# Kernel optimization log

Measured on AMD Instinct MI355X. Metric: run time of the kernel, lower is better.

The kernel has to match this reference:

```python
import jax, jax.numpy as jnp
import numpy as np

N_NODES = 50000
N_EDGES = 800000
IN_DIM = 256
HID_DIM = 128  # hidden_dim == output_dim (fc2 is applied twice in the original)


def setup_inputs() -> dict:
    key = jax.random.key(0)
    ks = jax.random.split(key, 8)
    x = jax.random.normal(ks[0], (N_NODES, IN_DIM), dtype=jnp.float32)
    W1 = jax.random.normal(ks[1], (IN_DIM, HID_DIM), dtype=jnp.float32) * (1.0 / np.sqrt(IN_DIM))
    b1 = jax.random.normal(ks[2], (HID_DIM,), dtype=jnp.float32) * 0.01
    W2 = jax.random.normal(ks[3], (HID_DIM, HID_DIM), dtype=jnp.float32) * (1.0 / np.sqrt(HID_DIM))
    b2 = jax.random.normal(ks[4], (HID_DIM,), dtype=jnp.float32) * 0.01
    adj_vals = jax.random.uniform(ks[5], (N_EDGES,), dtype=jnp.float32)
    adj_rows = jax.random.randint(ks[6], (N_EDGES,), 0, N_NODES, dtype=jnp.int32)
    adj_cols = jax.random.randint(ks[7], (N_EDGES,), 0, N_NODES, dtype=jnp.int32)
    return {"x": x, "W1": W1, "b1": b1, "W2": W2, "b2": b2,
            "adj_vals": adj_vals, "adj_rows": adj_rows, "adj_cols": adj_cols}


def reference(x, W1, b1, W2, b2, adj_vals, adj_rows, adj_cols):
    # fc1 + ReLU: [N, in] -> [N, hid]
    h = jax.nn.relu(x @ W1 + b1)
    # spmm(adj, h): out[i] = sum over edges (i<-j) vals * h[j]
    msgs = adj_vals[:, None] * h[adj_cols]            # [E, hid] gather
    agg = jax.ops.segment_sum(msgs, adj_rows, num_segments=N_NODES)  # [N, hid]
    # gcn_forward applies fc2, then forward applies fc2 AGAIN (faithful to source)
    h2 = agg @ W2 + b2
    logits = h2 @ W2 + b2
    return jax.nn.softmax(logits, axis=1)
```

## Files before the change

### kernel.cpp

```cpp
#include <hip/hip_runtime.h>
#include <hip/hip_fp16.h>

#define NN 50000
#define EE 800000
#define IND 256
#define HD 128
#define EPB 4096
#define GBLK 196
#define NBIN 196

typedef _Float16 half2v __attribute__((ext_vector_type(2)));
typedef _Float16 half4v __attribute__((ext_vector_type(4)));
typedef _Float16 half8v __attribute__((ext_vector_type(8)));
typedef float f32x4 __attribute__((ext_vector_type(4)));

__global__ __launch_bounds__(128) void w1t_kernel(const float* __restrict__ W1,
                                                  _Float16* __restrict__ W1T) {
  const int k = blockIdx.x;
  const int c = threadIdx.x;
  W1T[c * IND + k] = (_Float16)W1[k * HD + c];
}

__global__ __launch_bounds__(128) void w2sq_kernel(const float* __restrict__ W2,
                                                   const float* __restrict__ b2,
                                                   _Float16* __restrict__ W2sqT,
                                                   float* __restrict__ b2eff) {
  const int r = blockIdx.x;
  const int c = threadIdx.x;
  float acc = 0.f;
#pragma unroll 8
  for (int k = 0; k < HD; ++k)
    acc = fmaf(W2[r * HD + k], W2[k * HD + c], acc);
  W2sqT[c * HD + r] = (_Float16)acc;
  if (r == 0) {
    float be = b2[c];
#pragma unroll 8
    for (int k = 0; k < HD; ++k)
      be = fmaf(b2[k], W2[k * HD + c], be);
    b2eff[c] = be;
  }
}

__global__ __launch_bounds__(256) void fc1_kernel(const float* __restrict__ x,
                                                  const _Float16* __restrict__ W1T,
                                                  const float* __restrict__ b1,
                                                  _Float16* __restrict__ h) {
  __shared__ _Float16 As[64 * 40];
  const int tid = threadIdx.x;
  const int l = tid & 63;
  const int w = tid >> 6;
  const int row0 = blockIdx.x * 64;
  const int lr = l & 15;
  const int lk = l >> 4;

  f32x4 acc[4][2];
#pragma unroll
  for (int mi = 0; mi < 4; ++mi)
#pragma unroll
    for (int ni = 0; ni < 2; ++ni) acc[mi][ni] = (f32x4){0.f, 0.f, 0.f, 0.f};

#pragma unroll 1
  for (int kt = 0; kt < 8; ++kt) {
    const int k0 = kt * 32;
    __syncthreads();
#pragma unroll
    for (int i = 0; i < 2; ++i) {
      const int f = tid + i * 256;
      const int row = f >> 3, kq = f & 7;
      const int rg = min(row0 + row, NN - 1);
      const float4 xv = *(const float4*)&x[(size_t)rg * IND + k0 + kq * 4];
      half4v hv = {(_Float16)xv.x, (_Float16)xv.y, (_Float16)xv.z, (_Float16)xv.w};
      *(half4v*)&As[row * 40 + kq * 4] = hv;
    }
    __syncthreads();
    const half8v b0 = *(const half8v*)&W1T[(size_t)(w * 32 + lr) * IND + k0 + lk * 8];
    const half8v b1f = *(const half8v*)&W1T[(size_t)(w * 32 + 16 + lr) * IND + k0 + lk * 8];
#pragma unroll
    for (int mi = 0; mi < 4; ++mi) {
      const half8v a = *(const half8v*)&As[(mi * 16 + lr) * 40 + lk * 8];
      acc[mi][0] = __builtin_amdgcn_mfma_f32_16x16x32_f16(a, b0, acc[mi][0], 0, 0, 0);
      acc[mi][1] = __builtin_amdgcn_mfma_f32_16x16x32_f16(a, b1f, acc[mi][1], 0, 0, 0);
    }
  }
  const float bias0 = b1[w * 32 + lr];
  const float bias1 = b1[w * 32 + 16 + lr];
#pragma unroll
  for (int mi = 0; mi < 4; ++mi) {
#pragma unroll
    for (int j = 0; j < 4; ++j) {
      const int rg = row0 + mi * 16 + lk * 4 + j;
      if (rg < NN) {
        h[(size_t)rg * HD + w * 32 + lr] = (_Float16)fmaxf(acc[mi][0][j] + bias0, 0.f);
        h[(size_t)rg * HD + w * 32 + 16 + lr] = (_Float16)fmaxf(acc[mi][1][j] + bias1, 0.f);
      }
    }
  }
}

__global__ void hist_kernel(const int* __restrict__ rows, int* __restrict__ counts) {
  int e = blockIdx.x * 256 + threadIdx.x;
  if (e < EE) atomicAdd(&counts[rows[e]], 1);
}

__device__ inline int wave_incl_scan(int v, int lane) {
#pragma unroll
  for (int off = 1; off < 64; off <<= 1) {
    int n = __shfl_up(v, off);
    if (lane >= off) v += n;
  }
  return v;
}

__global__ __launch_bounds__(256) void scan_a_kernel(const int* __restrict__ counts,
                                                     int* __restrict__ incl,
                                                     int* __restrict__ bsum) {
  __shared__ int wtot[4];
  const int t = threadIdx.x;
  const int i = blockIdx.x * 256 + t;
  const int lane = t & 63, wid = t >> 6;
  const int v = (i < NN) ? counts[i] : 0;
  int sc = wave_incl_scan(v, lane);
  if (lane == 63) wtot[wid] = sc;
  __syncthreads();
  int pre = 0;
#pragma unroll
  for (int w = 0; w < 3; ++w) pre += (wid > w) ? wtot[w] : 0;
  if (i < NN) incl[i] = sc + pre;
  if (t == 255) bsum[blockIdx.x] = pre + sc;
}

__global__ __launch_bounds__(256) void scan_b_kernel(int* __restrict__ bsum,
                                                     int* __restrict__ boffs,
                                                     int nblk) {
  __shared__ int wtot[4];
  const int t = threadIdx.x;
  const int lane = t & 63, wid = t >> 6;
  const int v = (t < nblk) ? bsum[t] : 0;
  int sc = wave_incl_scan(v, lane);
  if (lane == 63) wtot[wid] = sc;
  __syncthreads();
  int pre = 0;
#pragma unroll
  for (int w = 0; w < 3; ++w) pre += (wid > w) ? wtot[w] : 0;
  if (t < nblk) boffs[t] = sc + pre - v;
}

__global__ __launch_bounds__(256) void scan_c_kernel(const int* __restrict__ incl,
                                                     const int* __restrict__ boffs,
                                                     int* __restrict__ row_ptr) {
  const int i = blockIdx.x * 256 + threadIdx.x;
  if (i == 0) row_ptr[0] = 0;
  if (i < NN) row_ptr[i + 1] = boffs[blockIdx.x] + incl[i];
}

__global__ __launch_bounds__(256) void count_kernel(const int* __restrict__ rows,
                                                    int* __restrict__ countmat) {
  __shared__ int cnt[NBIN];
  const int t = threadIdx.x, blk = blockIdx.x;
  for (int i = t; i < NBIN; i += 256) cnt[i] = 0;
  __syncthreads();
  const int e0 = blk * EPB;
  const int eN = min(e0 + EPB, EE);
  for (int e = e0 + t; e < eN; e += 256) atomicAdd(&cnt[rows[e] >> 8], 1);
  __syncthreads();
  for (int i = t; i < NBIN; i += 256) countmat[i * GBLK + blk] = cnt[i];
}

__global__ __launch_bounds__(256) void scanmat_kernel(const int* __restrict__ countmat,
                                                      const int* __restrict__ row_ptr,
                                                      int* __restrict__ offmat) {
  __shared__ int wtot[4];
  const int bin = blockIdx.x;
  const int t = threadIdx.x, lane = t & 63, wid = t >> 6;
  const int v = (t < GBLK) ? countmat[bin * GBLK + t] : 0;
  int sc = wave_incl_scan(v, lane);
  if (lane == 63) wtot[wid] = sc;
  __syncthreads();
  int pre = 0;
#pragma unroll
  for (int w = 0; w < 3; ++w) pre += (wid > w) ? wtot[w] : 0;
  const int binbase = row_ptr[bin << 8];
  if (t < GBLK) offmat[bin * GBLK + t] = binbase + pre + sc - v;
}

__global__ __launch_bounds__(256) void scatter_kernel(const int* __restrict__ rows,
                                                      const int* __restrict__ cols,
                                                      const float* __restrict__ vals,
                                                      const int* __restrict__ offmat,
                                                      uint2* __restrict__ edges_b) {
  __shared__ uint2 st[EPB];
  __shared__ unsigned char binof[EPB];
  __shared__ int cnt[NBIN], lofs[NBIN], gbase[NBIN];
  __shared__ int wtot[4];
  const int t = threadIdx.x, blk = blockIdx.x;
  const int lane = t & 63, wid = t >> 6;
  for (int i = t; i < NBIN; i += 256) cnt[i] = 0;
  __syncthreads();
  const int e0 = blk * EPB;
  const int n = min(EPB, EE - e0);
  for (int i = t; i < n; i += 256) atomicAdd(&cnt[rows[e0 + i] >> 8], 1);
  __syncthreads();
  {
    const int v = (t < NBIN) ? cnt[t] : 0;
    int sc = wave_incl_scan(v, lane);
    if (lane == 63) wtot[wid] = sc;
    __syncthreads();
    int pre = 0;
#pragma unroll
    for (int w = 0; w < 3; ++w) pre += (wid > w) ? wtot[w] : 0;
    if (t < NBIN) {
      lofs[t] = pre + sc - v;
      gbase[t] = offmat[t * GBLK + blk];
    }
  }
  __syncthreads();
  for (int i = t; i < NBIN; i += 256) cnt[i] = 0;
  __syncthreads();
  for (int i = t; i < n; i += 256) {
    const int r = rows[e0 + i];
    const int b = r >> 8;
    const int p = atomicAdd(&cnt[b], 1);
    const int j = lofs[b] + p;
    st[j] = make_uint2(__float_as_uint(vals[e0 + i]),
                       ((unsigned)r << 16) | (unsigned)cols[e0 + i]);
    binof[j] = (unsigned char)b;
  }
  __syncthreads();
  for (int j = t; j < n; j += 256) {
    const int b = binof[j];
    edges_b[gbase[b] + (j - lofs[b])] = st[j];
  }
}

__global__ __launch_bounds__(256) void binsort_kernel(const uint2* __restrict__ edges_b,
                                                      const int* __restrict__ row_ptr,
                                                      uint2* __restrict__ edges_s) {
  __shared__ int cur[256];
  const int bin = blockIdx.x;
  const int n0 = bin << 8;
  const int nEnd = min(n0 + 256, NN);
  const int t = threadIdx.x;
  if (n0 + t < nEnd) cur[t] = row_ptr[n0 + t];
  __syncthreads();
  const int s = row_ptr[n0];
  const int eEnd = row_ptr[nEnd];
  for (int i = s + t; i < eEnd; i += 256) {
    const uint2 ed = edges_b[i];
    const int r = (int)(ed.y >> 16);
    const int pos = atomicAdd(&cur[r & 255], 1);
    edges_s[pos] = make_uint2(ed.x, ed.y & 0xFFFFu);
  }
}

__global__ __launch_bounds__(256) void spmm_kernel(const _Float16* __restrict__ h,
                                                   const uint2* __restrict__ edges,
                                                   const int* __restrict__ row_ptr,
                                                   _Float16* __restrict__ agg16) {
  const int wid = threadIdx.x >> 6;
  const int lane = threadIdx.x & 63;
  const int node = blockIdx.x * 4 + wid;
  if (node >= NN) return;
  const int s = row_ptr[node];
  const int e = row_ptr[node + 1];
  const unsigned* __restrict__ hu = (const unsigned*)h;
  float ax = 0.f, ay = 0.f;
  int t = s;
  for (; t + 3 < e; t += 4) {
    const uint2 e0 = edges[t + 0], e1 = edges[t + 1];
    const uint2 e2 = edges[t + 2], e3 = edges[t + 3];
    const unsigned g0 = hu[(size_t)e0.y * 64 + lane];
    const unsigned g1 = hu[(size_t)e1.y * 64 + lane];
    const unsigned g2 = hu[(size_t)e2.y * 64 + lane];
    const unsigned g3 = hu[(size_t)e3.y * 64 + lane];
    const __half2 h0 = *(const __half2*)&g0;
    const __half2 h1 = *(const __half2*)&g1;
    const __half2 h2 = *(const __half2*)&g2;
    const __half2 h3 = *(const __half2*)&g3;
    const float v0 = __uint_as_float(e0.x), v1 = __uint_as_float(e1.x);
    const float v2 = __uint_as_float(e2.x), v3 = __uint_as_float(e3.x);
    ax = fmaf(v0, __low2float(h0), ax); ay = fmaf(v0, __high2float(h0), ay);
    ax = fmaf(v1, __low2float(h1), ax); ay = fmaf(v1, __high2float(h1), ay);
    ax = fmaf(v2, __low2float(h2), ax); ay = fmaf(v2, __high2float(h2), ay);
    ax = fmaf(v3, __low2float(h3), ax); ay = fmaf(v3, __high2float(h3), ay);
  }
  for (; t < e; ++t) {
    const uint2 ee = edges[t];
    const unsigned g = hu[(size_t)ee.y * 64 + lane];
    const __half2 hh = *(const __half2*)&g;
    const float v = __uint_as_float(ee.x);
    ax = fmaf(v, __low2float(hh), ax); ay = fmaf(v, __high2float(hh), ay);
  }
  half2v o = {(_Float16)ax, (_Float16)ay};
  *(half2v*)&agg16[(size_t)node * HD + lane * 2] = o;
}

__global__ __launch_bounds__(256) void fc2sm_kernel(const _Float16* __restrict__ agg16,
                                                    const _Float16* __restrict__ W2sqT,
                                                    const float* __restrict__ b2eff,
                                                    float* __restrict__ out) {
  __shared__ _Float16 As[64 * 136];
  __shared__ float redm[64][4];
  __shared__ float reds[64][4];
  const int tid = threadIdx.x;
  const int l = tid & 63;
  const int w = tid >> 6;
  const int row0 = blockIdx.x * 64;
  const int lr = l & 15;
  const int lk = l >> 4;

#pragma unroll
  for (int i = 0; i < 4; ++i) {
    const int f = tid + i * 256;
    const int row = f >> 4, q = f & 15;
    const int rg = min(row0 + row, NN - 1);
    *(uint4*)&As[row * 136 + q * 8] = *(const uint4*)&agg16[(size_t)rg * HD + q * 8];
  }
  __syncthreads();

  f32x4 acc[4][2];
#pragma unroll
  for (int mi = 0; mi < 4; ++mi)
#pragma unroll
    for (int ni = 0; ni < 2; ++ni) acc[mi][ni] = (f32x4){0.f, 0.f, 0.f, 0.f};

#pragma unroll 2
  for (int kt = 0; kt < 4; ++kt) {
    const int k0 = kt * 32;
    const half8v b0 = *(const half8v*)&W2sqT[(size_t)(w * 32 + lr) * HD + k0 + lk * 8];
    const half8v b1f = *(const half8v*)&W2sqT[(size_t)(w * 32 + 16 + lr) * HD + k0 + lk * 8];
#pragma unroll
    for (int mi = 0; mi < 4; ++mi) {
      const half8v a = *(const half8v*)&As[(mi * 16 + lr) * 136 + k0 + lk * 8];
      acc[mi][0] = __builtin_amdgcn_mfma_f32_16x16x32_f16(a, b0, acc[mi][0], 0, 0, 0);
      acc[mi][1] = __builtin_amdgcn_mfma_f32_16x16x32_f16(a, b1f, acc[mi][1], 0, 0, 0);
    }
  }

  const float be0 = b2eff[w * 32 + lr];
  const float be1 = b2eff[w * 32 + 16 + lr];
#pragma unroll
  for (int mi = 0; mi < 4; ++mi)
#pragma unroll
    for (int j = 0; j < 4; ++j) {
      acc[mi][0][j] += be0;
      acc[mi][1][j] += be1;
    }
#pragma unroll
  for (int mi = 0; mi < 4; ++mi)
#pragma unroll
    for (int j = 0; j < 4; ++j) {
      float v = fmaxf(acc[mi][0][j], acc[mi][1][j]);
      v = fmaxf(v, __shfl_xor(v, 1));
      v = fmaxf(v, __shfl_xor(v, 2));
      v = fmaxf(v, __shfl_xor(v, 4));
      v = fmaxf(v, __shfl_xor(v, 8));
      if (lr == 0) redm[mi * 16 + lk * 4 + j][w] = v;
    }
  __syncthreads();
#pragma unroll
  for (int mi = 0; mi < 4; ++mi)
#pragma unroll
    for (int j = 0; j < 4; ++j) {
      const int row = mi * 16 + lk * 4 + j;
      const float m = fmaxf(fmaxf(redm[row][0], redm[row][1]),
                            fmaxf(redm[row][2], redm[row][3]));
      const float e0 = __expf(acc[mi][0][j] - m);
      const float e1 = __expf(acc[mi][1][j] - m);
      acc[mi][0][j] = e0;
      acc[mi][1][j] = e1;
      float s = e0 + e1;
      s += __shfl_xor(s, 1);
      s += __shfl_xor(s, 2);
      s += __shfl_xor(s, 4);
      s += __shfl_xor(s, 8);
      if (lr == 0) reds[row][w] = s;
    }
  __syncthreads();
#pragma unroll
  for (int mi = 0; mi < 4; ++mi)
#pragma unroll
    for (int j = 0; j < 4; ++j) {
      const int row = mi * 16 + lk * 4 + j;
      const int rg = row0 + row;
      if (rg < NN) {
        const float inv = 1.f / (((reds[row][0] + reds[row][1]) +
                                  (reds[row][2] + reds[row][3])));
        out[(size_t)rg * HD + w * 32 + lr] = acc[mi][0][j] * inv;
        out[(size_t)rg * HD + w * 32 + 16 + lr] = acc[mi][1][j] * inv;
      }
    }
}

extern "C" void kernel_launch(void* const* d_in, const int* in_sizes, int n_in,
                              void* d_out, int out_size, void* d_ws, size_t ws_size,
                              hipStream_t stream) {
  (void)in_sizes; (void)n_in; (void)out_size; (void)ws_size;
  const float* x   = (const float*)d_in[0];
  const float* W1  = (const float*)d_in[1];
  const float* b1  = (const float*)d_in[2];
  const float* W2  = (const float*)d_in[3];
  const float* b2  = (const float*)d_in[4];
  const float* adj_vals = (const float*)d_in[5];
  const int* adj_rows   = (const int*)d_in[6];
  const int* adj_cols   = (const int*)d_in[7];
  float* out = (float*)d_out;

  char* ws = (char*)d_ws;
  _Float16* h      = (_Float16*)ws;
  _Float16* agg16  = (_Float16*)(ws + 12800000);
  _Float16* W1T    = (_Float16*)(ws + 25600000);
  _Float16* W2sqT  = (_Float16*)(ws + 25665536);
  float* b2eff     = (float*)(ws + 25698304);
  int* row_ptr     = (int*)(ws + 25698816);
  int* counts      = (int*)(ws + 25898880);
  int* incl        = (int*)(ws + 26098944);
  int* bsum        = (int*)(ws + 26299008);
  int* boffs       = (int*)(ws + 26300032);
  int* countmat    = (int*)(ws + 26301056);
  int* offmat      = (int*)(ws + 26454720);
  uint2* edges_b   = (uint2*)(ws + 26608384);
  uint2* edges_s   = (uint2*)(ws + 33008384);

  const int nblk = (NN + 255) / 256;

  hipMemsetAsync(counts, 0, NN * sizeof(int), stream);

  w1t_kernel<<<IND, HD, 0, stream>>>(W1, W1T);
  w2sq_kernel<<<HD, HD, 0, stream>>>(W2, b2, W2sqT, b2eff);
  fc1_kernel<<<(NN + 63) / 64, 256, 0, stream>>>(x, W1T, b1, h);
  hist_kernel<<<(EE + 255) / 256, 256, 0, stream>>>(adj_rows, counts);
  scan_a_kernel<<<nblk, 256, 0, stream>>>(counts, incl, bsum);
  scan_b_kernel<<<1, 256, 0, stream>>>(bsum, boffs, nblk);
  scan_c_kernel<<<nblk, 256, 0, stream>>>(incl, boffs, row_ptr);
  count_kernel<<<GBLK, 256, 0, stream>>>(adj_rows, countmat);
  scanmat_kernel<<<NBIN, 256, 0, stream>>>(countmat, row_ptr, offmat);
  scatter_kernel<<<GBLK, 256, 0, stream>>>(adj_rows, adj_cols, adj_vals, offmat, edges_b);
  binsort_kernel<<<NBIN, 256, 0, stream>>>(edges_b, row_ptr, edges_s);
  spmm_kernel<<<(NN + 3) / 4, 256, 0, stream>>>(h, edges_s, row_ptr, agg16);
  fc2sm_kernel<<<(NN + 63) / 64, 256, 0, stream>>>(agg16, W2sqT, b2eff, out);
}
```

Measured before the change: 254.5 us.

## Replace full CSR build with 64-row bins and LDS-atomic binned SpMM

Drops the per-node histogram, three-stage scan and the second bin-sort pass. Edges are now bucketed only into 64-row bins (782 bins), using a two-level scan of per-block counts. A new SpMM kernel processes one bin per block and accumulates into a 64x128 fp32 shared-memory tile with LDS atomics, keyed by the local row stored in the packed edge word. This removes several kernel launches and a full edge-array read/write pass, at the cost of shared-memory float atomics in the aggregation, which may contend and add float-ordering nondeterminism.

New measurement: 850.1 us. 234% more time.

```diff
diff --git a/kernel.cpp b/kernel.cpp
--- a/kernel.cpp
+++ b/kernel.cpp
@@ -7,7 +7,7 @@
 #define HD 128
 #define EPB 4096
 #define GBLK 196
-#define NBIN 196
+#define NB 782
 
 typedef _Float16 half2v __attribute__((ext_vector_type(2)));
 typedef _Float16 half4v __attribute__((ext_vector_type(4)));
@@ -97,11 +97,6 @@
   }
 }
 
-__global__ void hist_kernel(const int* __restrict__ rows, int* __restrict__ counts) {
-  int e = blockIdx.x * 256 + threadIdx.x;
-  if (e < EE) atomicAdd(&counts[rows[e]], 1);
-}
-
 __device__ inline int wave_incl_scan(int v, int lane) {
 #pragma unroll
   for (int off = 1; off < 64; off <<= 1) {
@@ -111,64 +106,22 @@
   return v;
 }
 
-__global__ __launch_bounds__(256) void scan_a_kernel(const int* __restrict__ counts,
-                                                     int* __restrict__ incl,
-                                                     int* __restrict__ bsum) {
-  __shared__ int wtot[4];
-  const int t = threadIdx.x;
-  const int i = blockIdx.x * 256 + t;
-  const int lane = t & 63, wid = t >> 6;
-  const int v = (i < NN) ? counts[i] : 0;
-  int sc = wave_incl_scan(v, lane);
-  if (lane == 63) wtot[wid] = sc;
-  __syncthreads();
-  int pre = 0;
-#pragma unroll
-  for (int w = 0; w < 3; ++w) pre += (wid > w) ? wtot[w] : 0;
-  if (i < NN) incl[i] = sc + pre;
-  if (t == 255) bsum[blockIdx.x] = pre + sc;
-}
-
-__global__ __launch_bounds__(256) void scan_b_kernel(int* __restrict__ bsum,
-                                                     int* __restrict__ boffs,
-                                                     int nblk) {
-  __shared__ int wtot[4];
-  const int t = threadIdx.x;
-  const int lane = t & 63, wid = t >> 6;
-  const int v = (t < nblk) ? bsum[t] : 0;
-  int sc = wave_incl_scan(v, lane);
-  if (lane == 63) wtot[wid] = sc;
-  __syncthreads();
-  int pre = 0;
-#pragma unroll
-  for (int w = 0; w < 3; ++w) pre += (wid > w) ? wtot[w] : 0;
-  if (t < nblk) boffs[t] = sc + pre - v;
-}
-
-__global__ __launch_bounds__(256) void scan_c_kernel(const int* __restrict__ incl,
-                                                     const int* __restrict__ boffs,
-                                                     int* __restrict__ row_ptr) {
-  const int i = blockIdx.x * 256 + threadIdx.x;
-  if (i == 0) row_ptr[0] = 0;
-  if (i < NN) row_ptr[i + 1] = boffs[blockIdx.x] + incl[i];
-}
-
 __global__ __launch_bounds__(256) void count_kernel(const int* __restrict__ rows,
                                                     int* __restrict__ countmat) {
-  __shared__ int cnt[NBIN];
+  __shared__ int cnt[NB];
   const int t = threadIdx.x, blk = blockIdx.x;
-  for (int i = t; i < NBIN; i += 256) cnt[i] = 0;
+  for (int i = t; i < NB; i += 256) cnt[i] = 0;
   __syncthreads();
   const int e0 = blk * EPB;
   const int eN = min(e0 + EPB, EE);
-  for (int e = e0 + t; e < eN; e += 256) atomicAdd(&cnt[rows[e] >> 8], 1);
-  __syncthreads();
-  for (int i = t; i < NBIN; i += 256) countmat[i * GBLK + blk] = cnt[i];
-}
-
-__global__ __launch_bounds__(256) void scanmat_kernel(const int* __restrict__ countmat,
-                                                      const int* __restrict__ row_ptr,
-                                                      int* __restrict__ offmat) {
+  for (int e = e0 + t; e < eN; e += 256) atomicAdd(&cnt[rows[e] >> 6], 1);
+  __syncthreads();
+  for (int i = t; i < NB; i += 256) countmat[i * GBLK + blk] = cnt[i];
+}
+
+__global__ __launch_bounds__(256) void scanwithin_kernel(const int* __restrict__ countmat,
+                                                         int* __restrict__ within,
+                                                         int* __restrict__ bintot) {
   __shared__ int wtot[4];
   const int bin = blockIdx.x;
   const int t = threadIdx.x, lane = t & 63, wid = t >> 6;
@@ -179,119 +132,131 @@
   int pre = 0;
 #pragma unroll
   for (int w = 0; w < 3; ++w) pre += (wid > w) ? wtot[w] : 0;
-  const int binbase = row_ptr[bin << 8];
-  if (t < GBLK) offmat[bin * GBLK + t] = binbase + pre + sc - v;
+  if (t < GBLK) within[bin * GBLK + t] = pre + sc - v;
+  if (t == 0) bintot[bin] = wtot[0] + wtot[1] + wtot[2] + wtot[3];
+}
+
+__global__ __launch_bounds__(1024) void binbase_kernel(const int* __restrict__ bintot,
+                                                       int* __restrict__ binstart) {
+  __shared__ int wtot[16];
+  const int t = threadIdx.x, lane = t & 63, wid = t >> 6;
+  const int v = (t < NB) ? bintot[t] : 0;
+  int sc = wave_incl_scan(v, lane);
+  if (lane == 63) wtot[wid] = sc;
+  __syncthreads();
+  if (wid == 0) {
+    int ws = (lane < 16) ? wtot[lane] : 0;
+    int wsc = wave_incl_scan(ws, lane);
+    if (lane < 16) wtot[lane] = wsc - ws;
+  }
+  __syncthreads();
+  const int incl = sc + wtot[wid];
+  if (t < NB) binstart[t + 1] = incl;
+  if (t == 0) binstart[0] = 0;
 }
 
 __global__ __launch_bounds__(256) void scatter_kernel(const int* __restrict__ rows,
                                                       const int* __restrict__ cols,
                                                       const float* __restrict__ vals,
-                                                      const int* __restrict__ offmat,
+                                                      const int* __restrict__ within,
+                                                      const int* __restrict__ binstart,
                                                       uint2* __restrict__ edges_b) {
   __shared__ uint2 st[EPB];
-  __shared__ unsigned char binof[EPB];
-  __shared__ int cnt[NBIN], lofs[NBIN], gbase[NBIN];
+  __shared__ unsigned short binof[EPB];
+  __shared__ int cnt[NB], lofs[NB], gb[NB];
   __shared__ int wtot[4];
   const int t = threadIdx.x, blk = blockIdx.x;
   const int lane = t & 63, wid = t >> 6;
-  for (int i = t; i < NBIN; i += 256) cnt[i] = 0;
+  for (int i = t; i < NB; i += 256) cnt[i] = 0;
   __syncthreads();
   const int e0 = blk * EPB;
   const int n = min(EPB, EE - e0);
-  for (int i = t; i < n; i += 256) atomicAdd(&cnt[rows[e0 + i] >> 8], 1);
+  for (int i = t; i < n; i += 256) atomicAdd(&cnt[rows[e0 + i] >> 6], 1);
   __syncthreads();
   {
-    const int v = (t < NBIN) ? cnt[t] : 0;
-    int sc = wave_incl_scan(v, lane);
+    const int i0 = t * 4;
+    const int v0 = (i0 + 0 < NB) ? cnt[i0 + 0] : 0;
+    const int v1 = (i0 + 1 < NB) ? cnt[i0 + 1] : 0;
+    const int v2 = (i0 + 2 < NB) ? cnt[i0 + 2] : 0;
+    const int v3 = (i0 + 3 < NB) ? cnt[i0 + 3] : 0;
+    const int s0 = v0, s1 = s0 + v1, s2 = s1 + v2, s3 = s2 + v3;
+    int sc = wave_incl_scan(s3, lane);
     if (lane == 63) wtot[wid] = sc;
     __syncthreads();
     int pre = 0;
 #pragma unroll
     for (int w = 0; w < 3; ++w) pre += (wid > w) ? wtot[w] : 0;
-    if (t < NBIN) {
-      lofs[t] = pre + sc - v;
-      gbase[t] = offmat[t * GBLK + blk];
-    }
-  }
-  __syncthreads();
-  for (int i = t; i < NBIN; i += 256) cnt[i] = 0;
+    const int excl = pre + sc - s3;
+    __syncthreads();
+    if (i0 + 0 < NB) { lofs[i0 + 0] = excl;      gb[i0 + 0] = binstart[i0 + 0] + within[(i0 + 0) * GBLK + blk]; }
+    if (i0 + 1 < NB) { lofs[i0 + 1] = excl + s0; gb[i0 + 1] = binstart[i0 + 1] + within[(i0 + 1) * GBLK + blk]; }
+    if (i0 + 2 < NB) { lofs[i0 + 2] = excl + s1; gb[i0 + 2] = binstart[i0 + 2] + within[(i0 + 2) * GBLK + blk]; }
+    if (i0 + 3 < NB) { lofs[i0 + 3] = excl + s2; gb[i0 + 3] = binstart[i0 + 3] + within[(i0 + 3) * GBLK + blk]; }
+  }
+  __syncthreads();
+  for (int i = t; i < NB; i += 256) cnt[i] = 0;
   __syncthreads();
   for (int i = t; i < n; i += 256) {
     const int r = rows[e0 + i];
-    const int b = r >> 8;
+    const int b = r >> 6;
     const int p = atomicAdd(&cnt[b], 1);
     const int j = lofs[b] + p;
     st[j] = make_uint2(__float_as_uint(vals[e0 + i]),
-                       ((unsigned)r << 16) | (unsigned)cols[e0 + i]);
-    binof[j] = (unsigned char)b;
+                       ((unsigned)(r & 63) << 16) | (unsigned)cols[e0 + i]);
+    binof[j] = (unsigned short)b;
   }
   __syncthreads();
   for (int j = t; j < n; j += 256) {
     const int b = binof[j];
-    edges_b[gbase[b] + (j - lofs[b])] = st[j];
-  }
-}
-
-__global__ __launch_bounds__(256) void binsort_kernel(const uint2* __restrict__ edges_b,
-                                                      const int* __restrict__ row_ptr,
-                                                      uint2* __restrict__ edges_s) {
-  __shared__ int cur[256];
-  const int bin = blockIdx.x;
-  const int n0 = bin << 8;
-  const int nEnd = min(n0 + 256, NN);
+    edges_b[gb[b] + (j - lofs[b])] = st[j];
+  }
+}
+
+__global__ __launch_bounds__(256) void spmm_bin_kernel(const _Float16* __restrict__ h,
+                                                       const uint2* __restrict__ edges_b,
+                                                       const int* __restrict__ binstart,
+                                                       _Float16* __restrict__ agg16) {
+  __shared__ float acc[64 * HD];
   const int t = threadIdx.x;
-  if (n0 + t < nEnd) cur[t] = row_ptr[n0 + t];
-  __syncthreads();
-  const int s = row_ptr[n0];
-  const int eEnd = row_ptr[nEnd];
-  for (int i = s + t; i < eEnd; i += 256) {
-    const uint2 ed = edges_b[i];
-    const int r = (int)(ed.y >> 16);
-    const int pos = atomicAdd(&cur[r & 255], 1);
-    edges_s[pos] = make_uint2(ed.x, ed.y & 0xFFFFu);
-  }
-}
-
-__global__ __launch_bounds__(256) void spmm_kernel(const _Float16* __restrict__ h,
-                                                   const uint2* __restrict__ edges,
-                                                   const int* __restrict__ row_ptr,
-                                                   _Float16* __restrict__ agg16) {
-  const int wid = threadIdx.x >> 6;
-  const int lane = threadIdx.x & 63;
-  const int node = blockIdx.x * 4 + wid;
-  if (node >= NN) return;
-  const int s = row_ptr[node];
-  const int e = row_ptr[node + 1];
+  const int w = t >> 6;
+  const int lane = t & 63;
+  const int b = blockIdx.x;
+  for (int i = t; i < 64 * HD / 4; i += 256) ((f32x4*)acc)[i] = (f32x4){0.f, 0.f, 0.f, 0.f};
+  __syncthreads();
+  const int s = binstart[b];
+  const int e = binstart[b + 1];
   const unsigned* __restrict__ hu = (const unsigned*)h;
-  float ax = 0.f, ay = 0.f;
-  int t = s;
-  for (; t + 3 < e; t += 4) {
-    const uint2 e0 = edges[t + 0], e1 = edges[t + 1];
-    const uint2 e2 = edges[t + 2], e3 = edges[t + 3];
-    const unsigned g0 = hu[(size_t)e0.y * 64 + lane];
-    const unsigned g1 = hu[(size_t)e1.y * 64 + lane];
-    const unsigned g2 = hu[(size_t)e2.y * 64 + lane];
-    const unsigned g3 = hu[(size_t)e3.y * 64 + lane];
-    const __half2 h0 = *(const __half2*)&g0;
-    const __half2 h1 = *(const __half2*)&g1;
-    const __half2 h2 = *(const __half2*)&g2;
-    const __half2 h3 = *(const __half2*)&g3;
-    const float v0 = __uint_as_float(e0.x), v1 = __uint_as_float(e1.x);
-    const float v2 = __uint_as_float(e2.x), v3 = __uint_as_float(e3.x);
-    ax = fmaf(v0, __low2float(h0), ax); ay = fmaf(v0, __high2float(h0), ay);
-    ax = fmaf(v1, __low2float(h1), ax); ay = fmaf(v1, __high2float(h1), ay);
-    ax = fmaf(v2, __low2float(h2), ax); ay = fmaf(v2, __high2float(h2), ay);
-    ax = fmaf(v3, __low2float(h3), ax); ay = fmaf(v3, __high2float(h3), ay);
-  }
-  for (; t < e; ++t) {
-    const uint2 ee = edges[t];
-    const unsigned g = hu[(size_t)ee.y * 64 + lane];
-    const __half2 hh = *(const __half2*)&g;
-    const float v = __uint_as_float(ee.x);
-    ax = fmaf(v, __low2float(hh), ax); ay = fmaf(v, __high2float(hh), ay);
-  }
-  half2v o = {(_Float16)ax, (_Float16)ay};
-  *(half2v*)&agg16[(size_t)node * HD + lane * 2] = o;
+#pragma unroll 1
+  for (int base = s + w * 4; base < e; base += 16) {
+    const int m = min(4, e - base);
+    uint2 ed[4];
+    unsigned g[4];
+#pragma unroll
+    for (int k = 0; k < 4; ++k)
+      if (k < m) {
+        ed[k] = edges_b[base + k];
+        g[k] = hu[(size_t)(ed[k].y & 0xFFFFu) * 64 + lane];
+      }
+#pragma unroll
+    for (int k = 0; k < 4; ++k)
+      if (k < m) {
+        const float v = __uint_as_float(ed[k].x);
+        const __half2 hh = *(const __half2*)&g[k];
+        const int r = (int)(ed[k].y >> 16);
+        atomicAdd(&acc[r * HD + lane * 2], v * __low2float(hh));
+        atomicAdd(&acc[r * HD + lane * 2 + 1], v * __high2float(hh));
+      }
+  }
+  __syncthreads();
+  for (int i = t; i < 64 * HD / 2; i += 256) {
+    const int row = i >> 6;
+    const int d = (i & 63) * 2;
+    const int node = b * 64 + row;
+    if (node < NN) {
+      half2v o = {(_Float16)acc[row * HD + d], (_Float16)acc[row * HD + d + 1]};
+      *(half2v*)&agg16[(size_t)node * HD + d] = o;
+    }
+  }
 }
 
 __global__ __launch_bounds__(256) void fc2sm_kernel(const _Float16* __restrict__ agg16,
@@ -411,31 +376,20 @@
   _Float16* W1T    = (_Float16*)(ws + 25600000);
   _Float16* W2sqT  = (_Float16*)(ws + 25665536);
   float* b2eff     = (float*)(ws + 25698304);
-  int* row_ptr     = (int*)(ws + 25698816);
-  int* counts      = (int*)(ws + 25898880);
-  int* incl        = (int*)(ws + 26098944);
-  int* bsum        = (int*)(ws + 26299008);
-  int* boffs       = (int*)(ws + 26300032);
-  int* countmat    = (int*)(ws + 26301056);
-  int* offmat      = (int*)(ws + 26454720);
-  uint2* edges_b   = (uint2*)(ws + 26608384);
-  uint2* edges_s   = (uint2*)(ws + 33008384);
-
-  const int nblk = (NN + 255) / 256;
-
-  hipMemsetAsync(counts, 0, NN * sizeof(int), stream);
+  int* binstart    = (int*)(ws + 25698816);
+  int* bintot      = (int*)(ws + 25702400);
+  int* countmat    = (int*)(ws + 25705536);
+  int* within      = (int*)(ws + 26318624);
+  uint2* edges_b   = (uint2*)(ws + 26931712);
 
   w1t_kernel<<<IND, HD, 0, stream>>>(W1, W1T);
   w2sq_kernel<<<HD, HD, 0, stream>>>(W2, b2, W2sqT, b2eff);
   fc1_kernel<<<(NN + 63) / 64, 256, 0, stream>>>(x, W1T, b1, h);
-  hist_kernel<<<(EE + 255) / 256, 256, 0, stream>>>(adj_rows, counts);
-  scan_a_kernel<<<nblk, 256, 0, stream>>>(counts, incl, bsum);
-  scan_b_kernel<<<1, 256, 0, stream>>>(bsum, boffs, nblk);
-  scan_c_kernel<<<nblk, 256, 0, stream>>>(incl, boffs, row_ptr);
   count_kernel<<<GBLK, 256, 0, stream>>>(adj_rows, countmat);
-  scanmat_kernel<<<NBIN, 256, 0, stream>>>(countmat, row_ptr, offmat);
-  scatter_kernel<<<GBLK, 256, 0, stream>>>(adj_rows, adj_cols, adj_vals, offmat, edges_b);
-  binsort_kernel<<<NBIN, 256, 0, stream>>>(edges_b, row_ptr, edges_s);
-  spmm_kernel<<<(NN + 3) / 4, 256, 0, stream>>>(h, edges_s, row_ptr, agg16);
+  scanwithin_kernel<<<NB, 256, 0, stream>>>(countmat, within, bintot);
+  binbase_kernel<<<1, 1024, 0, stream>>>(bintot, binstart);
+  scatter_kernel<<<GBLK, 256, 0, stream>>>(adj_rows, adj_cols, adj_vals,
+                                           within, binstart, edges_b);
+  spmm_bin_kernel<<<NB, 256, 0, stream>>>(h, edges_b, binstart, agg16);
   fc2sm_kernel<<<(NN + 63) / 64, 256, 0, stream>>>(agg16, W2sqT, b2eff, out);
 }
```
